# Performance work log

Hardware: AMD Instinct MI355X
Metric: run time of the kernel (lower is better)

Reference implementation:

```python
import jax, jax.numpy as jnp
import numpy as np

N = 50000      # nodes
E = 800000     # edges (avg degree 16)
D_IN = 128
D_H = 128
D_OUT = 64
SLOPE = 0.2    # leaky-relu negative slope (from the 0.2 constants in the graph)


def setup_inputs() -> dict:
    key = jax.random.key(0)
    ks = jax.random.split(key, 18)
    def w(k, shape, fan_in):
        return jax.random.normal(k, shape, jnp.float32) / np.sqrt(fan_in)
    inp = {
        "x": jax.random.normal(ks[0], (N, D_IN), jnp.float32),
        "W0": w(ks[1], (D_IN, D_H), D_IN),
        "b0": jnp.zeros((D_H,), jnp.float32),
        "Wq1": w(ks[2], (D_H, D_H), D_H),
        "bq1": jnp.zeros((D_H,), jnp.float32),
        "Wp1": w(ks[3], (D_H, D_H), D_H),
        "bp1": jnp.zeros((D_H,), jnp.float32),
        "a1": 0.1 * w(ks[4], (D_H,), D_H),
        "bg2": jnp.zeros((D_H,), jnp.float32),
        "Wq2": w(ks[5], (D_H, D_OUT), D_H),
        "bq2": jnp.zeros((D_OUT,), jnp.float32),
        "Wp2": w(ks[6], (D_H, D_OUT), D_H),
        "bp2": jnp.zeros((D_OUT,), jnp.float32),
        "a2": 0.1 * w(ks[7], (D_OUT,), D_OUT),
        "b_out": jnp.zeros((D_OUT,), jnp.float32),
        "src": jax.random.randint(ks[8], (E,), 0, N),
        "dst": jax.random.randint(ks[9], (E,), 0, N),
        "num_nodes": N,
    }
    return inp


def _gat_block(m, src, dst, Wq, bq, Wp, bp, a, n):
    # m: [N, d_in]; q/p: [N, d]
    q = m @ Wq + bq
    p = m @ Wp + bp
    # edge scores: s_e = sum_d leaky_relu(q[dst_e] + p[src_e]) * a_d   [E]
    e = jax.nn.leaky_relu(q[dst] + p[src], SLOPE)          # [E, d]
    s = jnp.einsum("ed,d->e", e, a)                        # [E]
    es = jnp.exp(s)                                        # unstabilized exp, as in source graph
    denom = jax.ops.segment_sum(es, dst, num_segments=n)   # [N]
    alpha = es / denom[dst]                                # [E] edge softmax over incoming edges
    # aggregate messages alpha_e * p[src_e] into dst nodes
    agg = jax.ops.segment_sum(alpha[:, None] * p[src], dst, num_segments=n)  # [N, d]
    return agg


def reference(x, W0, b0, Wq1, bq1, Wp1, bp1, a1, bg2, Wq2, bq2, Wp2, bp2, a2, b_out, src, dst, num_nodes):
    m1 = jax.nn.gelu(x @ W0 + b0, approximate=False)       # erf GELU per graph constants
    h1 = _gat_block(m1, src, dst, Wq1, bq1, Wp1, bp1, a1, num_nodes)
    m2 = jax.nn.gelu(h1 + bg2, approximate=False)
    h2 = _gat_block(m2, src, dst, Wq2, bq2, Wp2, bp2, a2, num_nodes)
    return h2 + b_out
```

## Files before the change

### kernel.cpp

```cpp
#include <hip/hip_runtime.h>
#include <hip/hip_bf16.h>
#include <math.h>


#define SLOPE 0.2f

typedef __attribute__((ext_vector_type(8))) __bf16 bf16x8;
typedef __attribute__((ext_vector_type(4))) float f32x4;

__device__ __forceinline__ float gelu_erf(float x) {
    return 0.5f * x * (1.0f + erff(x * 0.70710678118654752f));
}

__device__ __forceinline__ unsigned short f2bf(float f) {
    unsigned int u = __float_as_uint(f);
    return (unsigned short)((u + 0x7fffu + ((u >> 16) & 1u)) >> 16);
}
__device__ __forceinline__ float bf2f(unsigned short h) {
    return __uint_as_float((unsigned int)h << 16);
}

__device__ __forceinline__ float row16_sum(float x) {
    x += __int_as_float(__builtin_amdgcn_update_dpp(0, __float_as_int(x), 0x121, 0xF, 0xF, true));
    x += __int_as_float(__builtin_amdgcn_update_dpp(0, __float_as_int(x), 0x122, 0xF, 0xF, true));
    x += __int_as_float(__builtin_amdgcn_update_dpp(0, __float_as_int(x), 0x124, 0xF, 0xF, true));
    x += __int_as_float(__builtin_amdgcn_update_dpp(0, __float_as_int(x), 0x128, 0xF, 0xF, true));
    return x;
}

__device__ __forceinline__ int swz(int off) { return off ^ ((off >> 4) & 0x70); }

__global__ __launch_bounds__(256) void pack_w(
    const float* __restrict__ W0,  const float* __restrict__ Wq1,
    const float* __restrict__ Wp1, const float* __restrict__ Wq2,
    const float* __restrict__ Wp2,
    unsigned short* __restrict__ P0,  unsigned short* __restrict__ Pq1,
    unsigned short* __restrict__ Pp1, unsigned short* __restrict__ Pq2,
    unsigned short* __restrict__ Pp2)
{
    const float* W; unsigned short* P; int C;
    switch (blockIdx.y) {
        case 0:  W = W0;  P = P0;  C = 128; break;
        case 1:  W = Wq1; P = Pq1; C = 128; break;
        case 2:  W = Wp1; P = Pp1; C = 128; break;
        case 3:  W = Wq2; P = Pq2; C = 64;  break;
        default: W = Wp2; P = Pp2; C = 64;  break;
    }
    int i = blockIdx.x * 256 + threadIdx.x;
    int CE = C * 128;
    if (i >= CE) return;
    int j = i & 7, l = (i >> 3) & 63, ks = (i >> 9) & 3, ct = i >> 11;
    int k = ks * 32 + ((l >> 4) << 3) + j;
    int n = ct * 16 + (l & 15);
    float v = W[k * C + n];
    unsigned short hb = f2bf(v);
    P[i] = hb;
    P[CE + i] = f2bf(v - bf2f(hb));
}

template <int C, bool TWO, int EPI>
__global__ __launch_bounds__(256) void mfma_gemm(
    const float* __restrict__ Af,
    const unsigned short* __restrict__ AHg, const unsigned short* __restrict__ ALg,
    const unsigned short* __restrict__ P1, const float* __restrict__ b1,
    const unsigned short* __restrict__ P2, const float* __restrict__ b2,
    float* __restrict__ outq, unsigned short* __restrict__ outp,
    unsigned short* __restrict__ o1hi, unsigned short* __restrict__ o1lo,
    int N)
{
    constexpr int CE  = C * 128;
    constexpr int CTT = (TWO ? 2 : 1) * (C / 16);
    constexpr int CTW = CTT / 4;
    constexpr int QCT = C / 16;

    __shared__ __align__(16) unsigned char lds[32768];

    const int t = threadIdx.x;
    const int lane = t & 63;
    const int w = t >> 6;
    const int row0 = blockIdx.x * 64;
    const int mcol = lane & 15;
    const int hk = lane >> 4;

    if constexpr (EPI == 0) {
#pragma unroll
        for (int i = 0; i < 8; i++) {
            int idx = t + i * 256;
            int row = idx >> 5;
            int gr = row0 + row;
            float4 v = make_float4(0.f, 0.f, 0.f, 0.f);
            if (gr < N) v = *reinterpret_cast<const float4*>(Af + (size_t)gr * 128 + (idx & 31) * 4);
            const float* f = reinterpret_cast<const float*>(&v);
            unsigned int h[4], l[4];
#pragma unroll
            for (int j = 0; j < 4; j++) {
                unsigned short hb = f2bf(f[j]);
                h[j] = hb;
                l[j] = f2bf(f[j] - bf2f(hb));
            }
            int so = swz(row * 256 + (idx & 31) * 8);
            *reinterpret_cast<uint2*>(&lds[so])         = make_uint2(h[0] | (h[1] << 16), h[2] | (h[3] << 16));
            *reinterpret_cast<uint2*>(&lds[16384 + so]) = make_uint2(l[0] | (l[1] << 16), l[2] | (l[3] << 16));
        }
    } else {
#pragma unroll
        for (int i = 0; i < 4; i++) {
            int idx = t + i * 256;
            int row = idx >> 4;
            int gr = row0 + row;
            uint4 vh = make_uint4(0, 0, 0, 0), vl = make_uint4(0, 0, 0, 0);
            if (gr < N) {
                vh = *reinterpret_cast<const uint4*>(AHg + (size_t)gr * 128 + (idx & 15) * 8);
                vl = *reinterpret_cast<const uint4*>(ALg + (size_t)gr * 128 + (idx & 15) * 8);
            }
            int so = swz(row * 256 + (idx & 15) * 16);
            *reinterpret_cast<uint4*>(&lds[so])         = vh;
            *reinterpret_cast<uint4*>(&lds[16384 + so]) = vl;
        }
    }
    __syncthreads();

    f32x4 acc[CTW][4];
#pragma unroll
    for (int c = 0; c < CTW; c++)
#pragma unroll
        for (int rf = 0; rf < 4; rf++) acc[c][rf] = (f32x4){0.f, 0.f, 0.f, 0.f};

#pragma unroll
    for (int ks = 0; ks < 4; ks++) {
        bf16x8 ah[4], al[4];
#pragma unroll
        for (int rf = 0; rf < 4; rf++) {
            int so = swz((rf * 16 + mcol) * 256 + ks * 64 + hk * 16);
            ah[rf] = *reinterpret_cast<const bf16x8*>(&lds[so]);
            al[rf] = *reinterpret_cast<const bf16x8*>(&lds[16384 + so]);
        }
#pragma unroll
        for (int c = 0; c < CTW; c++) {
            int ctg = w * CTW + c;
            bool isq = (!TWO) || (ctg < QCT);
            int ct = isq ? ctg : ctg - QCT;
            const unsigned short* P = isq ? P1 : P2;
            const unsigned short* Wp = P + ((ct * 4 + ks) * 64 + lane) * 8;
            bf16x8 bh = *reinterpret_cast<const bf16x8*>(Wp);
            bf16x8 bl = *reinterpret_cast<const bf16x8*>(Wp + CE);
#pragma unroll
            for (int rf = 0; rf < 4; rf++) {
                acc[c][rf] = __builtin_amdgcn_mfma_f32_16x16x32_bf16(ah[rf], bh, acc[c][rf], 0, 0, 0);
                acc[c][rf] = __builtin_amdgcn_mfma_f32_16x16x32_bf16(al[rf], bh, acc[c][rf], 0, 0, 0);
                acc[c][rf] = __builtin_amdgcn_mfma_f32_16x16x32_bf16(ah[rf], bl, acc[c][rf], 0, 0, 0);
            }
        }
    }

    __syncthreads();

    if constexpr (EPI == 0) {
#pragma unroll
        for (int c = 0; c < CTW; c++) {
            int col = (w * CTW + c) * 16 + mcol;
            float bv = b1[col];
#pragma unroll
            for (int rf = 0; rf < 4; rf++) {
#pragma unroll
                for (int r = 0; r < 4; r++) {
                    int row = rf * 16 + hk * 4 + r;
                    float v = gelu_erf(acc[c][rf][r] + bv);
                    unsigned short hb = f2bf(v);
                    int bo = row * 256 + col * 2;
                    *reinterpret_cast<unsigned short*>(&lds[swz(bo)])         = hb;
                    *reinterpret_cast<unsigned short*>(&lds[16384 + swz(bo)]) = f2bf(v - bf2f(hb));
                }
            }
        }
        __syncthreads();
#pragma unroll
        for (int i = 0; i < 8; i++) {
            int idx = t + i * 256;
            int pl = idx >> 10;
            int j = idx & 1023;
            int row = j >> 4;
            int gr = row0 + row;
            if (gr < N) {
                uint4 v = *reinterpret_cast<const uint4*>(&lds[pl * 16384 + swz(row * 256 + (j & 15) * 16)]);
                unsigned short* dp = pl ? o1lo : o1hi;
                *reinterpret_cast<uint4*>(dp + (size_t)gr * 128 + (j & 15) * 8) = v;
            }
        }
    } else {
#pragma unroll
        for (int c = 0; c < CTW; c++) {
            int ctg = w * CTW + c;
            bool isq = ctg < QCT;
            int ct = isq ? ctg : ctg - QCT;
            int col = ct * 16 + mcol;
            float bv = (isq ? b1 : b2)[col];
#pragma unroll
            for (int rf = 0; rf < 4; rf++) {
#pragma unroll
                for (int r = 0; r < 4; r++) {
                    int row = rf * 16 + hk * 4 + r;
                    int gr = row0 + row;
                    float v = acc[c][rf][r] + bv;
                    if (isq) {
                        if (gr < N) outq[(size_t)gr * C + col] = v;
                    } else {
                        *reinterpret_cast<unsigned short*>(&lds[swz(row * 256 + col * 2)]) = f2bf(v);
                    }
                }
            }
        }
        __syncthreads();
        constexpr int SLOTS = C / 8;
#pragma unroll
        for (int i = 0; i < (64 * SLOTS) / 256; i++) {
            int idx = t + i * 256;
            int row = idx / SLOTS;
            int sl = idx % SLOTS;
            int gr = row0 + row;
            if (gr < N)
                *reinterpret_cast<uint4*>(outp + (size_t)gr * C + sl * 8) =
                    *reinterpret_cast<const uint4*>(&lds[swz(row * 256 + sl * 16)]);
        }
    }
}


__global__ __launch_bounds__(256) void hist_coarse(
    const int* __restrict__ dst, int* __restrict__ gh, int E, int CB)
{
    __shared__ int cnt[4096];
    const int blk = blockIdx.x;
    const int t = threadIdx.x;
    for (int b = t; b < CB; b += 256) cnt[b] = 0;
    __syncthreads();
    const int epb = (E + 63) / 64;
    const int s = blk * epb;
    const int e_ = (s + epb < E) ? s + epb : E;
    for (int i = s + t; i < e_; i += 256)
        atomicAdd(&cnt[dst[i] >> 4], 1);
    __syncthreads();
    for (int b = t; b < CB; b += 256)
        gh[b * 64 + blk] = cnt[b];
}

__global__ __launch_bounds__(256) void scan1_kernel(const int* __restrict__ gh,
                                                    int* __restrict__ gscan,
                                                    int* __restrict__ bsum, int M)
{
    __shared__ int lds[256];
    int t = threadIdx.x;
    int i = blockIdx.x * 256 + t;
    int v = (i < M) ? gh[i] : 0;
    lds[t] = v;
    __syncthreads();
    int x = v;
    for (int off = 1; off < 256; off <<= 1) {
        int y = (t >= off) ? lds[t - off] : 0;
        __syncthreads();
        x += y;
        lds[t] = x;
        __syncthreads();
    }
    if (i < M) gscan[i] = x - v;
    if (t == 255) bsum[blockIdx.x] = x;
}

__global__ __launch_bounds__(1024) void scan2_kernel(int* __restrict__ bsum, int NB)
{
    __shared__ int lds[1024];
    int t = threadIdx.x;
    int v = (t < NB) ? bsum[t] : 0;
    lds[t] = v;
    __syncthreads();
    int x = v;
    for (int off = 1; off < 1024; off <<= 1) {
        int y = (t >= off) ? lds[t - off] : 0;
        __syncthreads();
        x += y;
        lds[t] = x;
        __syncthreads();
    }
    if (t < NB) bsum[t] = x - v;
}

__global__ __launch_bounds__(256) void scan3_kernel(int* __restrict__ gscan,
                                                    const int* __restrict__ bsum, int M)
{
    int i = blockIdx.x * 256 + threadIdx.x;
    if (i < M) gscan[i] += bsum[blockIdx.x];
}

__global__ __launch_bounds__(256) void scatter_coarse(
    const int* __restrict__ src, const int* __restrict__ dst,
    const int* __restrict__ gscan, int2* __restrict__ pairs, int E, int CB)
{
    __shared__ int cur[4096];
    const int blk = blockIdx.x;
    const int t = threadIdx.x;
    for (int b = t; b < CB; b += 256)
        cur[b] = gscan[b * 64 + blk];
    __syncthreads();
    const int epb = (E + 63) / 64;
    const int s = blk * epb;
    const int e_ = (s + epb < E) ? s + epb : E;
    for (int i = s + t; i < e_; i += 256) {
        int d = dst[i];
        int sv = src[i];
        int pos = atomicAdd(&cur[d >> 4], 1);
        pairs[pos] = make_int2(d, sv);
    }
}

__global__ __launch_bounds__(256) void finalize_kernel(
    const int2* __restrict__ pairs, const int* __restrict__ gscan,
    int* __restrict__ offs, int* __restrict__ csr_src, int N, int E, int CB)
{
    const int wid = blockIdx.x * 4 + (threadIdx.x >> 6);
    const int lane = threadIdx.x & 63;
    if (wid >= CB) return;

    const int s    = gscan[wid * 64];
    const int e_   = (wid + 1 < CB) ? gscan[(wid + 1) * 64] : E;
    const int base = wid * 16;
    const unsigned long long ltmask = (lane == 63) ? ~0ull >> 1
                                                   : (1ull << lane) - 1ull;

    int rc[16];
#pragma unroll
    for (int j = 0; j < 16; j++) rc[j] = 0;
    for (int c0 = s; c0 < e_; c0 += 64) {
        int i = c0 + lane;
        int d = (i < e_) ? pairs[i].x - base : -1;
#pragma unroll
        for (int j = 0; j < 16; j++)
            rc[j] += (int)__popcll(__ballot(d == j));
    }

    int pref[16];
    int run = s;
#pragma unroll
    for (int j = 0; j < 16; j++) { pref[j] = run; run += rc[j]; }
    int pref_v = 0;
#pragma unroll
    for (int j = 0; j < 16; j++) pref_v = (lane == j) ? pref[j] : pref_v;

    if (lane < 16 && base + lane < N) offs[base + lane] = pref_v;
    if (wid == CB - 1 && lane == 16) offs[N] = E;

    int rcv = 0;
    for (int c0 = s; c0 < e_; c0 += 64) {
        int i = c0 + lane;
        const bool act = i < e_;
        int2 pr = act ? pairs[i] : make_int2(base - 1, 0);
        int d = pr.x - base;
        unsigned long long msel = 0;
        int addcnt = 0;
#pragma unroll
        for (int j = 0; j < 16; j++) {
            unsigned long long m = __ballot(d == j);
            if (d == j) msel = m;
            if (lane == j) addcnt = (int)__popcll(m);
        }
        int subrank = (int)__popcll(msel & ltmask);
        int posbase = __builtin_amdgcn_ds_bpermute(d * 4, pref_v + rcv);
        if (act) csr_src[posbase + subrank] = pr.y;
        rcv += addcnt;
    }
}

template <int D, int EPI>
__global__ __launch_bounds__(256) void gat_agg(
    const float* __restrict__ q, const unsigned short* __restrict__ p,
    const float* __restrict__ a, const float* __restrict__ bvec,
    const int* __restrict__ offs, const int* __restrict__ csr_src,
    float* __restrict__ out, unsigned short* __restrict__ mhi,
    unsigned short* __restrict__ mlo, int N)
{
    constexpr int VPL = D / 16;
    const int t = threadIdx.x;
    const int lane = t & 63;
    const int sl = lane & 15;
    const int base = sl * VPL;
    const int node = blockIdx.x * 16 + ((t >> 6) << 2) + (lane >> 4);
    const bool valid = node < N;

    float qv[VPL], a6[VPL], a4[VPL], acc[VPL];
#pragma unroll
    for (int v = 0; v < VPL; v++) { qv[v] = 0.f; acc[v] = 0.f; }
    if (valid) {
        const float* qp = q + (size_t)node * D + base;
        float4 q0 = *reinterpret_cast<const float4*>(qp);
        qv[0] = q0.x; qv[1] = q0.y; qv[2] = q0.z; qv[3] = q0.w;
        if constexpr (VPL == 8) {
            float4 q1 = *reinterpret_cast<const float4*>(qp + 4);
            qv[4] = q1.x; qv[5] = q1.y; qv[6] = q1.z; qv[7] = q1.w;
        }
    }
#pragma unroll
    for (int v = 0; v < VPL; v++) {
        float av = a[base + v];
        a6[v] = 0.6f * av;
        a4[v] = 0.4f * av;
    }

    auto gather = [&](int s) -> uint4 {
        if constexpr (D == 128) {
            return *reinterpret_cast<const uint4*>(p + (size_t)s * 128 + base);
        } else {
            uint2 u = *reinterpret_cast<const uint2*>(p + (size_t)s * 64 + base);
            return make_uint4(u.x, u.y, 0u, 0u);
        }
    };
    auto unpack = [&](uint4 u, float* pv) {
        pv[0] = __uint_as_float(u.x << 16); pv[1] = __uint_as_float(u.x & 0xffff0000u);
        pv[2] = __uint_as_float(u.y << 16); pv[3] = __uint_as_float(u.y & 0xffff0000u);
        if constexpr (VPL == 8) {
            pv[4] = __uint_as_float(u.z << 16); pv[5] = __uint_as_float(u.z & 0xffff0000u);
            pv[6] = __uint_as_float(u.w << 16); pv[7] = __uint_as_float(u.w & 0xffff0000u);
        }
    };

    float denom = 0.f;
    int e  = valid ? offs[node] : 0;
    int e1 = valid ? offs[node + 1] : 0;

    int s0 = csr_src[(e + 0 < e1) ? e + 0 : 0];
    int s1 = csr_src[(e + 1 < e1) ? e + 1 : 0];
    int s2 = csr_src[(e + 2 < e1) ? e + 2 : 0];
    int s3 = csr_src[(e + 3 < e1) ? e + 3 : 0];
    uint4 uA0 = gather(s0), uA1 = gather(s1), uA2 = gather(s2), uA3 = gather(s3);
    int en = e + 4;
    int n0 = csr_src[(en + 0 < e1) ? en + 0 : 0];
    int n1 = csr_src[(en + 1 < e1) ? en + 1 : 0];
    int n2 = csr_src[(en + 2 < e1) ? en + 2 : 0];
    int n3 = csr_src[(en + 3 < e1) ? en + 3 : 0];

    while (__any(e < e1)) {
        const bool a0 = (e + 0) < e1, a1b = (e + 1) < e1,
                   a2 = (e + 2) < e1, a3 = (e + 3) < e1;

        uint4 v0 = gather(n0), v1 = gather(n1), v2 = gather(n2), v3 = gather(n3);

        const int em = en + 4;
        const int m0 = csr_src[(em + 0 < e1) ? em + 0 : 0];
        const int m1 = csr_src[(em + 1 < e1) ? em + 1 : 0];
        const int m2 = csr_src[(em + 2 < e1) ? em + 2 : 0];
        const int m3 = csr_src[(em + 3 < e1) ? em + 3 : 0];

        float pv[4][VPL];
        unpack(uA0, pv[0]); unpack(uA1, pv[1]); unpack(uA2, pv[2]); unpack(uA3, pv[3]);

        float pa0 = 0.f, pa1 = 0.f, pa2 = 0.f, pa3 = 0.f;
#pragma unroll
        for (int v = 0; v < VPL; v++) {
            float d0 = qv[v] + pv[0][v];
            float d1 = qv[v] + pv[1][v];
            float d2 = qv[v] + pv[2][v];
            float d3 = qv[v] + pv[3][v];
            pa0 = fmaf(d0, a6[v], pa0); pa0 = fmaf(fabsf(d0), a4[v], pa0);
            pa1 = fmaf(d1, a6[v], pa1); pa1 = fmaf(fabsf(d1), a4[v], pa1);
            pa2 = fmaf(d2, a6[v], pa2); pa2 = fmaf(fabsf(d2), a4[v], pa2);
            pa3 = fmaf(d3, a6[v], pa3); pa3 = fmaf(fabsf(d3), a4[v], pa3);
        }

        float r0 = row16_sum(pa0);
        float r1 = row16_sum(pa1);
        float r2 = row16_sum(pa2);
        float r3 = row16_sum(pa3);

        float esm0 = a0  ? __expf(r0) : 0.f;
        float esm1 = a1b ? __expf(r1) : 0.f;
        float esm2 = a2  ? __expf(r2) : 0.f;
        float esm3 = a3  ? __expf(r3) : 0.f;
        denom += (esm0 + esm1) + (esm2 + esm3);
#pragma unroll
        for (int v = 0; v < VPL; v++) {
            acc[v] = fmaf(esm0, pv[0][v], acc[v]);
            acc[v] = fmaf(esm1, pv[1][v], acc[v]);
            acc[v] = fmaf(esm2, pv[2][v], acc[v]);
            acc[v] = fmaf(esm3, pv[3][v], acc[v]);
        }

        uA0 = v0; uA1 = v1; uA2 = v2; uA3 = v3;
        n0 = m0; n1 = m1; n2 = m2; n3 = m3;
        e = en; en = em;
    }

    if (!valid) return;
    float inv = (denom != 0.f) ? 1.f / denom : 0.f;
    if constexpr (EPI == 0) {
        union { unsigned short us[8]; uint4 v; } H, L;
#pragma unroll
        for (int v = 0; v < VPL; v++) {
            float g = gelu_erf(acc[v] * inv + bvec[base + v]);
            H.us[v] = f2bf(g);
            L.us[v] = f2bf(g - bf2f(H.us[v]));
        }
        *reinterpret_cast<uint4*>(mhi + (size_t)node * 128 + base) = H.v;
        *reinterpret_cast<uint4*>(mlo + (size_t)node * 128 + base) = L.v;
    } else {
        union { float f[4]; float4 v; } O;
#pragma unroll
        for (int v = 0; v < VPL; v++) O.f[v] = acc[v] * inv + bvec[base + v];
        *reinterpret_cast<float4*>(out + (size_t)node * D + base) = O.v;
    }
}

extern "C" void kernel_launch(void* const* d_in, const int* in_sizes, int n_in,
                              void* d_out, int out_size, void* d_ws, size_t ws_size,
                              hipStream_t stream)
{
    const float* x     = (const float*)d_in[0];
    const float* W0    = (const float*)d_in[1];
    const float* b0    = (const float*)d_in[2];
    const float* Wq1   = (const float*)d_in[3];
    const float* bq1   = (const float*)d_in[4];
    const float* Wp1   = (const float*)d_in[5];
    const float* bp1   = (const float*)d_in[6];
    const float* a1    = (const float*)d_in[7];
    const float* bg2   = (const float*)d_in[8];
    const float* Wq2   = (const float*)d_in[9];
    const float* bq2   = (const float*)d_in[10];
    const float* Wp2   = (const float*)d_in[11];
    const float* bp2   = (const float*)d_in[12];
    const float* a2    = (const float*)d_in[13];
    const float* b_out = (const float*)d_in[14];
    const int*   src   = (const int*)d_in[15];
    const int*   dst   = (const int*)d_in[16];

    const int N = in_sizes[0] / 128;
    const int E = in_sizes[15];
    float* out = (float*)d_out;

    float* q_buf        = (float*)d_ws;
    unsigned short* pb  = (unsigned short*)(q_buf + (size_t)N * 128);
    unsigned short* Mhi = pb + (size_t)N * 128;
    unsigned short* Mlo = Mhi + (size_t)N * 128;
    unsigned short* P0  = Mlo + (size_t)N * 128;
    unsigned short* Pq1 = P0  + 128 * 128 * 2;
    unsigned short* Pp1 = Pq1 + 128 * 128 * 2;
    unsigned short* Pq2 = Pp1 + 128 * 128 * 2;
    unsigned short* Pp2 = Pq2 + 128 * 64 * 2;
    int* offs    = (int*)(Pp2 + 128 * 64 * 2);
    int* csr_src = offs + (N + 2);
    const int CB = (N + 15) / 16;
    const int M  = CB * 64;
    int* gh    = csr_src + E;
    int* gscan = gh + M;
    int* bsum  = gscan + M;
    int2* pairs = (int2*)q_buf;

    const int NB1 = (M + 255) / 256;

    pack_w<<<dim3(64, 5), 256, 0, stream>>>(W0, Wq1, Wp1, Wq2, Wp2,
                                            P0, Pq1, Pp1, Pq2, Pp2);
    hist_coarse<<<64, 256, 0, stream>>>(dst, gh, E, CB);
    scan1_kernel<<<NB1, 256, 0, stream>>>(gh, gscan, bsum, M);
    scan2_kernel<<<1, 1024, 0, stream>>>(bsum, NB1);
    scan3_kernel<<<NB1, 256, 0, stream>>>(gscan, bsum, M);
    scatter_coarse<<<64, 256, 0, stream>>>(src, dst, gscan, pairs, E, CB);
    finalize_kernel<<<(CB + 3) / 4, 256, 0, stream>>>(pairs, gscan, offs, csr_src, N, E, CB);

    const int GB64 = (N + 63) / 64;
    const int GGAT = (N + 15) / 16;

    mfma_gemm<128, false, 0><<<GB64, 256, 0, stream>>>(
        x, nullptr, nullptr, P0, b0, nullptr, nullptr,
        nullptr, nullptr, Mhi, Mlo, N);
    mfma_gemm<128, true, 1><<<GB64, 256, 0, stream>>>(
        nullptr, Mhi, Mlo, Pq1, bq1, Pp1, bp1,
        q_buf, pb, nullptr, nullptr, N);
    gat_agg<128, 0><<<GGAT, 256, 0, stream>>>(
        q_buf, pb, a1, bg2, offs, csr_src,
        nullptr, Mhi, Mlo, N);
    mfma_gemm<64, true, 1><<<GB64, 256, 0, stream>>>(
        nullptr, Mhi, Mlo, Pq2, bq2, Pp2, bp2,
        q_buf, pb, nullptr, nullptr, N);
    gat_agg<64, 1><<<GGAT, 256, 0, stream>>>(
        q_buf, pb, a2, b_out, offs, csr_src,
        out, nullptr, nullptr, N);
}
```

Before: 283.6 us.

## Fuse CSR construction kernels into one cooperative grid-synced kernel

Replaces the histogram, three-stage scan, scatter and finalize kernels with a single cooperative kernel of 64 blocks that separates phases with grid syncs. The scan is restructured so each block scans a contiguous chunk with per-thread serial prefixes. This removes several kernel launches and their inter-kernel gaps, but the finalize phase now runs on only 64 blocks and each grid sync adds its own cost.

```diff
diff --git a/kernel.cpp b/kernel.cpp
--- a/kernel.cpp
+++ b/kernel.cpp
@@ -1,6 +1,9 @@
 #include <hip/hip_runtime.h>
 #include <hip/hip_bf16.h>
+#include <hip/hip_cooperative_groups.h>
 #include <math.h>
+
+namespace cg = cooperative_groups;
 
 
 #define SLOPE 0.2f
@@ -225,147 +228,153 @@
     }
 }
 
-
-__global__ __launch_bounds__(256) void hist_coarse(
-    const int* __restrict__ dst, int* __restrict__ gh, int E, int CB)
+__global__ __launch_bounds__(256) void csr_build(
+    const int* __restrict__ src, const int* __restrict__ dst,
+    int* __restrict__ gh, int* __restrict__ gscan, int* __restrict__ bsum,
+    int2* __restrict__ pairs, int* __restrict__ offs, int* __restrict__ csr_src,
+    int N, int E, int CB)
 {
-    __shared__ int cnt[4096];
+    cg::grid_group grid = cg::this_grid();
+    __shared__ int smem[4096];
     const int blk = blockIdx.x;
     const int t = threadIdx.x;
-    for (int b = t; b < CB; b += 256) cnt[b] = 0;
+    const int lane = t & 63;
+    const int M = CB * 64;
+
+    for (int b = t; b < CB; b += 256) smem[b] = 0;
     __syncthreads();
     const int epb = (E + 63) / 64;
-    const int s = blk * epb;
-    const int e_ = (s + epb < E) ? s + epb : E;
-    for (int i = s + t; i < e_; i += 256)
-        atomicAdd(&cnt[dst[i] >> 4], 1);
+    const int es = blk * epb;
+    const int ee = (es + epb < E) ? es + epb : E;
+    for (int i = es + t; i < ee; i += 256)
+        atomicAdd(&smem[dst[i] >> 4], 1);
     __syncthreads();
     for (int b = t; b < CB; b += 256)
-        gh[b * 64 + blk] = cnt[b];
-}
-
-__global__ __launch_bounds__(256) void scan1_kernel(const int* __restrict__ gh,
-                                                    int* __restrict__ gscan,
-                                                    int* __restrict__ bsum, int M)
-{
-    __shared__ int lds[256];
-    int t = threadIdx.x;
-    int i = blockIdx.x * 256 + t;
-    int v = (i < M) ? gh[i] : 0;
-    lds[t] = v;
-    __syncthreads();
-    int x = v;
+        gh[b * 64 + blk] = smem[b];
+    __threadfence();
+    grid.sync();
+
+    const int chunk = (M + 63) / 64;
+    const int c0 = blk * chunk;
+    const int c1 = (c0 + chunk < M) ? c0 + chunk : M;
+    const int cpt = (chunk + 255) / 256;
+    const int bi = c0 + t * cpt;
+    int vals[16];
+    int tsum = 0;
+#pragma unroll
+    for (int j = 0; j < 16; j++) {
+        if (j < cpt) {
+            int i = bi + j;
+            int v = (i < c1) ? gh[i] : 0;
+            vals[j] = tsum;
+            tsum += v;
+        }
+    }
+    __syncthreads();
+    smem[t] = tsum;
+    __syncthreads();
+    int x = tsum;
     for (int off = 1; off < 256; off <<= 1) {
-        int y = (t >= off) ? lds[t - off] : 0;
+        int y = (t >= off) ? smem[t - off] : 0;
         __syncthreads();
         x += y;
-        lds[t] = x;
+        smem[t] = x;
         __syncthreads();
     }
-    if (i < M) gscan[i] = x - v;
-    if (t == 255) bsum[blockIdx.x] = x;
-}
-
-__global__ __launch_bounds__(1024) void scan2_kernel(int* __restrict__ bsum, int NB)
-{
-    __shared__ int lds[1024];
-    int t = threadIdx.x;
-    int v = (t < NB) ? bsum[t] : 0;
-    lds[t] = v;
-    __syncthreads();
-    int x = v;
-    for (int off = 1; off < 1024; off <<= 1) {
-        int y = (t >= off) ? lds[t - off] : 0;
+    const int tpref = x - tsum;
+    if (t == 255) bsum[blk] = x;
+    __threadfence();
+    grid.sync();
+
+    if (blk == 0) {
+        int v = (t < 64) ? bsum[t] : 0;
+        smem[t] = v;
         __syncthreads();
-        x += y;
-        lds[t] = x;
-        __syncthreads();
-    }
-    if (t < NB) bsum[t] = x - v;
-}
-
-__global__ __launch_bounds__(256) void scan3_kernel(int* __restrict__ gscan,
-                                                    const int* __restrict__ bsum, int M)
-{
-    int i = blockIdx.x * 256 + threadIdx.x;
-    if (i < M) gscan[i] += bsum[blockIdx.x];
-}
-
-__global__ __launch_bounds__(256) void scatter_coarse(
-    const int* __restrict__ src, const int* __restrict__ dst,
-    const int* __restrict__ gscan, int2* __restrict__ pairs, int E, int CB)
-{
-    __shared__ int cur[4096];
-    const int blk = blockIdx.x;
-    const int t = threadIdx.x;
+        int x2 = v;
+        for (int off = 1; off < 64; off <<= 1) {
+            int y = (t >= off && t < 64) ? smem[t - off] : 0;
+            __syncthreads();
+            x2 += y;
+            smem[t] = x2;
+            __syncthreads();
+        }
+        if (t < 64) bsum[t] = x2 - v;
+        __threadfence();
+    }
+    grid.sync();
+
+    const int boff = bsum[blk];
+#pragma unroll
+    for (int j = 0; j < 16; j++) {
+        if (j < cpt) {
+            int i = bi + j;
+            if (i < c1) gscan[i] = boff + tpref + vals[j];
+        }
+    }
+    __threadfence();
+    grid.sync();
+
+    __syncthreads();
     for (int b = t; b < CB; b += 256)
-        cur[b] = gscan[b * 64 + blk];
-    __syncthreads();
-    const int epb = (E + 63) / 64;
-    const int s = blk * epb;
-    const int e_ = (s + epb < E) ? s + epb : E;
-    for (int i = s + t; i < e_; i += 256) {
+        smem[b] = gscan[b * 64 + blk];
+    __syncthreads();
+    for (int i = es + t; i < ee; i += 256) {
         int d = dst[i];
         int sv = src[i];
-        int pos = atomicAdd(&cur[d >> 4], 1);
+        int pos = atomicAdd(&smem[d >> 4], 1);
         pairs[pos] = make_int2(d, sv);
     }
-}
-
-__global__ __launch_bounds__(256) void finalize_kernel(
-    const int2* __restrict__ pairs, const int* __restrict__ gscan,
-    int* __restrict__ offs, int* __restrict__ csr_src, int N, int E, int CB)
-{
-    const int wid = blockIdx.x * 4 + (threadIdx.x >> 6);
-    const int lane = threadIdx.x & 63;
-    if (wid >= CB) return;
-
-    const int s    = gscan[wid * 64];
-    const int e_   = (wid + 1 < CB) ? gscan[(wid + 1) * 64] : E;
-    const int base = wid * 16;
+    __threadfence();
+    grid.sync();
+
     const unsigned long long ltmask = (lane == 63) ? ~0ull >> 1
                                                    : (1ull << lane) - 1ull;
-
-    int rc[16];
-#pragma unroll
-    for (int j = 0; j < 16; j++) rc[j] = 0;
-    for (int c0 = s; c0 < e_; c0 += 64) {
-        int i = c0 + lane;
-        int d = (i < e_) ? pairs[i].x - base : -1;
-#pragma unroll
-        for (int j = 0; j < 16; j++)
-            rc[j] += (int)__popcll(__ballot(d == j));
-    }
-
-    int pref[16];
-    int run = s;
-#pragma unroll
-    for (int j = 0; j < 16; j++) { pref[j] = run; run += rc[j]; }
-    int pref_v = 0;
-#pragma unroll
-    for (int j = 0; j < 16; j++) pref_v = (lane == j) ? pref[j] : pref_v;
-
-    if (lane < 16 && base + lane < N) offs[base + lane] = pref_v;
-    if (wid == CB - 1 && lane == 16) offs[N] = E;
-
-    int rcv = 0;
-    for (int c0 = s; c0 < e_; c0 += 64) {
-        int i = c0 + lane;
-        const bool act = i < e_;
-        int2 pr = act ? pairs[i] : make_int2(base - 1, 0);
-        int d = pr.x - base;
-        unsigned long long msel = 0;
-        int addcnt = 0;
-#pragma unroll
-        for (int j = 0; j < 16; j++) {
-            unsigned long long m = __ballot(d == j);
-            if (d == j) msel = m;
-            if (lane == j) addcnt = (int)__popcll(m);
-        }
-        int subrank = (int)__popcll(msel & ltmask);
-        int posbase = __builtin_amdgcn_ds_bpermute(d * 4, pref_v + rcv);
-        if (act) csr_src[posbase + subrank] = pr.y;
-        rcv += addcnt;
+    for (int wid = blk * 4 + (t >> 6); wid < CB; wid += 256) {
+        const int s    = gscan[wid * 64];
+        const int e_   = (wid + 1 < CB) ? gscan[(wid + 1) * 64] : E;
+        const int base = wid * 16;
+
+        int rc[16];
+#pragma unroll
+        for (int j = 0; j < 16; j++) rc[j] = 0;
+        for (int cc = s; cc < e_; cc += 64) {
+            int i = cc + lane;
+            int d = (i < e_) ? pairs[i].x - base : -1;
+#pragma unroll
+            for (int j = 0; j < 16; j++)
+                rc[j] += (int)__popcll(__ballot(d == j));
+        }
+
+        int pref[16];
+        int run = s;
+#pragma unroll
+        for (int j = 0; j < 16; j++) { pref[j] = run; run += rc[j]; }
+        int pref_v = 0;
+#pragma unroll
+        for (int j = 0; j < 16; j++) pref_v = (lane == j) ? pref[j] : pref_v;
+
+        if (lane < 16 && base + lane < N) offs[base + lane] = pref_v;
+        if (wid == CB - 1 && lane == 16) offs[N] = E;
+
+        int rcv = 0;
+        for (int cc = s; cc < e_; cc += 64) {
+            int i = cc + lane;
+            const bool act = i < e_;
+            int2 pr = act ? pairs[i] : make_int2(base - 1, 0);
+            int d = pr.x - base;
+            unsigned long long msel = 0;
+            int addcnt = 0;
+#pragma unroll
+            for (int j = 0; j < 16; j++) {
+                unsigned long long m = __ballot(d == j);
+                if (d == j) msel = m;
+                if (lane == j) addcnt = (int)__popcll(m);
+            }
+            int subrank = (int)__popcll(msel & ltmask);
+            int posbase = __builtin_amdgcn_ds_bpermute(d * 4, pref_v + rcv);
+            if (act) csr_src[posbase + subrank] = pr.y;
+            rcv += addcnt;
+        }
     }
 }
 
@@ -551,16 +560,17 @@
     int* bsum  = gscan + M;
     int2* pairs = (int2*)q_buf;
 
-    const int NB1 = (M + 255) / 256;
-
     pack_w<<<dim3(64, 5), 256, 0, stream>>>(W0, Wq1, Wp1, Wq2, Wp2,
                                             P0, Pq1, Pp1, Pq2, Pp2);
-    hist_coarse<<<64, 256, 0, stream>>>(dst, gh, E, CB);
-    scan1_kernel<<<NB1, 256, 0, stream>>>(gh, gscan, bsum, M);
-    scan2_kernel<<<1, 1024, 0, stream>>>(bsum, NB1);
-    scan3_kernel<<<NB1, 256, 0, stream>>>(gscan, bsum, M);
-    scatter_coarse<<<64, 256, 0, stream>>>(src, dst, gscan, pairs, E, CB);
-    finalize_kernel<<<(CB + 3) / 4, 256, 0, stream>>>(pairs, gscan, offs, csr_src, N, E, CB);
+    {
+        void* args[] = {
+            (void*)&src, (void*)&dst, (void*)&gh, (void*)&gscan, (void*)&bsum,
+            (void*)&pairs, (void*)&offs, (void*)&csr_src,
+            (void*)&N, (void*)&E, (void*)&CB
+        };
+        hipLaunchCooperativeKernel((const void*)csr_build, dim3(64), dim3(256),
+                                   args, 0, stream);
+    }
 
     const int GB64 = (N + 63) / 64;
     const int GGAT = (N + 15) / 16;
```

New measurement: 445.5 us. +57.1%, slower.
